# Kernel optimization log

Hardware: AMD Instinct MI355X
Metric: run time of the kernel (lower is better)

Reference implementation:

```python
import jax, jax.numpy as jnp
import numpy as np

N = 131072      # total nodes
E = 262144      # directed edges (~2 per node, molecular graphs)
B = 4096        # number of graphs
D = 300         # emb_dim
L = 5           # num_layer
MAXN = 96       # max nodes per graph (static cap)
NUM_ATOM, NUM_CHI = 120, 3
NUM_BOND, NUM_DIR = 6, 3   # bond type vocab incl. self-loop id 4; bond direction
BN_EPS = 1e-5
SELF_LOOP_BOND = 4


def setup_inputs() -> dict:
    key = jax.random.key(0)
    ks = jax.random.split(key, 24)
    s = 1.0 / np.sqrt(D)
    x = jnp.stack([jax.random.randint(ks[0], (N,), 0, NUM_ATOM),
                   jax.random.randint(ks[1], (N,), 0, NUM_CHI)], axis=1)
    edge_index = jax.random.randint(ks[2], (2, E), 0, N)
    edge_attr = jnp.stack([jax.random.randint(ks[3], (E,), 0, 4),
                           jax.random.randint(ks[4], (E,), 0, NUM_DIR)], axis=1)
    batch = jnp.sort(jax.random.randint(ks[5], (N,), 0, B)).at[-1].set(B - 1)
    return dict(
        x=x, edge_index=edge_index, edge_attr=edge_attr, batch=batch, max_nodes=MAXN,
        atom_emb1=jax.random.normal(ks[6], (NUM_ATOM, D)) * s,
        atom_emb2=jax.random.normal(ks[7], (NUM_CHI, D)) * s,
        edge_emb1=jax.random.normal(ks[8], (L, NUM_BOND, D)) * s,
        edge_emb2=jax.random.normal(ks[9], (L, NUM_DIR, D)) * s,
        W1=jax.random.normal(ks[10], (L, D, 2 * D)) * s,
        b1=jnp.zeros((L, 2 * D)),
        W2=jax.random.normal(ks[11], (L, 2 * D, D)) * (1.0 / np.sqrt(2 * D)),
        b2=jnp.zeros((L, D)),
        bn_gamma=jax.random.uniform(ks[12], (L, D), minval=0.8, maxval=1.2),
        bn_beta=jax.random.normal(ks[13], (L, D)) * 0.05,
        bn_mean=jax.random.normal(ks[14], (L, D)) * 0.05,
        bn_var=jax.random.uniform(ks[15], (L, D), minval=0.5, maxval=1.5),
    )


def reference(x, edge_index, edge_attr, batch, max_nodes,
              atom_emb1, atom_emb2, edge_emb1, edge_emb2,
              W1, b1, W2, b2, bn_gamma, bn_beta, bn_mean, bn_var):
    n = x.shape[0]
    # add self-loops with edge_attr [SELF_LOOP_BOND, 0] (chem GIN convention)
    loops = jnp.arange(n, dtype=edge_index.dtype)
    src = jnp.concatenate([edge_index[0], loops])
    dst = jnp.concatenate([edge_index[1], loops])
    sl = jnp.stack([jnp.full((n,), SELF_LOOP_BOND, edge_attr.dtype),
                    jnp.zeros((n,), edge_attr.dtype)], axis=1)
    ea = jnp.concatenate([edge_attr, sl], axis=0)

    h = atom_emb1[x[:, 0]] + atom_emb2[x[:, 1]]  # [N, D]
    for l in range(L):
        e = edge_emb1[l][ea[:, 0]] + edge_emb2[l][ea[:, 1]]     # [E+N, D]
        msg = h[src] + e                                         # gather + add
        agg = jax.ops.segment_sum(msg, dst, num_segments=n)      # scatter-add
        h = jnp.maximum(agg @ W1[l] + b1[l], 0.0) @ W2[l] + b2[l]  # GIN MLP
        h = bn_gamma[l] * (h - bn_mean[l]) * jax.lax.rsqrt(bn_var[l] + BN_EPS) + bn_beta[l]
        if l < L - 1:
            h = jnp.maximum(h, 0.0)

    # ragged -> dense pack (replaces the per-graph python copy loop)
    counts = jax.ops.segment_sum(jnp.ones((n,), jnp.int32), batch, num_segments=B)
    offsets = jnp.concatenate([jnp.zeros((1,), counts.dtype), jnp.cumsum(counts)[:-1]])
    pos = jnp.arange(n, dtype=counts.dtype) - offsets[batch]     # within-graph index
    padded = jnp.zeros((B, max_nodes, h.shape[1]), h.dtype).at[batch, pos].set(h)
    padding_mask = jnp.arange(max_nodes)[None, :] >= counts[:, None]
    return padded, padding_mask
```

## Files before the change

kernel.cpp:

```cpp
#include <hip/hip_runtime.h>

typedef _Float16 f16;
typedef __attribute__((ext_vector_type(8))) _Float16 f16x8;
typedef __attribute__((ext_vector_type(4))) float f32x4;

#define D_      300
#define DP      320
#define L_      5
#define MAXN_   96
#define NGRAPH  4096
#define MAXDEG  32

__global__ void k_prep_w(const float* __restrict__ W1, const float* __restrict__ W2,
                         f16* __restrict__ W1t, f16* __restrict__ W2t) {
  const int T1 = L_ * 640 * 320;
  const int T2 = L_ * 304 * 640;
  for (int idx = blockIdx.x * blockDim.x + threadIdx.x; idx < T1 + T2;
       idx += gridDim.x * blockDim.x) {
    if (idx < T1) {
      int l = idx / (640 * 320), r = idx % (640 * 320);
      int j = r / 320, k = r % 320;
      W1t[idx] = (j < 600 && k < 300) ? (f16)W1[(l * 300 + k) * 600 + j] : (f16)0.0f;
    } else {
      int i2 = idx - T1;
      int l = i2 / (304 * 640), r = i2 % (304 * 640);
      int c = r / 640, k = r % 640;
      W2t[i2] = (c < 300 && k < 600) ? (f16)W2[(l * 600 + k) * 300 + c] : (f16)0.0f;
    }
  }
}

__global__ void k_prep_eemb(const float* __restrict__ ee1, const float* __restrict__ ee2,
                            float* __restrict__ eemb) {
  int total = L_ * 13 * 304;
  for (int idx = blockIdx.x * blockDim.x + threadIdx.x; idx < total;
       idx += gridDim.x * blockDim.x) {
    int l = idx / (13 * 304), r = idx % (13 * 304);
    int c = r / 304, d = r % 304;
    int bond = (c == 12) ? 4 : (c / 3);
    int dir  = (c == 12) ? 0 : (c % 3);
    eemb[idx] = (d < 300) ? ee1[(l * 6 + bond) * 300 + d] + ee2[(l * 3 + dir) * 300 + d]
                          : 0.0f;
  }
}

__global__ void k_bc_init(int* counts, int* offsets) {
  int i = blockIdx.x * blockDim.x + threadIdx.x;
  if (i < NGRAPH) { counts[i] = 0; offsets[i] = 0x7fffffff; }
}
__global__ void k_zero_i32(int* p, int n) {
  for (int i = blockIdx.x * blockDim.x + threadIdx.x; i < n; i += gridDim.x * blockDim.x)
    p[i] = 0;
}
__global__ void k_bc_count(const int* __restrict__ batch, int n, int* counts, int* offsets) {
  int i = blockIdx.x * blockDim.x + threadIdx.x;
  if (i < n) { int b = batch[i]; atomicAdd(&counts[b], 1); atomicMin(&offsets[b], i); }
}
__global__ void k_pos(const int* __restrict__ batch, const int* __restrict__ offsets,
                      int n, int* __restrict__ pos) {
  int i = blockIdx.x * blockDim.x + threadIdx.x;
  if (i < n) pos[i] = i - offsets[batch[i]];
}
__global__ void k_mask(const int* __restrict__ counts, float* __restrict__ mask) {
  int i = blockIdx.x * blockDim.x + threadIdx.x;
  if (i < NGRAPH * MAXN_) {
    int b = i / MAXN_, j = i % MAXN_;
    mask[i] = (j >= counts[b]) ? 1.0f : 0.0f;
  }
}
__global__ void k_zero(uint4* __restrict__ p, long nchunks) {
  for (long i = blockIdx.x * (long)blockDim.x + threadIdx.x; i < nchunks;
       i += (long)gridDim.x * blockDim.x)
    p[i] = make_uint4(0u, 0u, 0u, 0u);
}

__global__ void k_epack(const int* __restrict__ src, const int* __restrict__ dst,
                        const int* __restrict__ ea, int ne,
                        int* __restrict__ deg, int* __restrict__ epack) {
  int e = blockIdx.x * blockDim.x + threadIdx.x;
  if (e < ne) {
    int t = dst[e];
    int p = atomicAdd(&deg[t], 1);
    if (p < MAXDEG) epack[t * MAXDEG + p] = src[e] | ((ea[2 * e] * 3 + ea[2 * e + 1]) << 17);
  }
}

__global__ void k_init_h(const int* __restrict__ x, const float* __restrict__ ae1,
                         const float* __restrict__ ae2, f16* __restrict__ h, int n) {
  long total = (long)n * DP;
  for (long idx = blockIdx.x * (long)blockDim.x + threadIdx.x; idx < total;
       idx += (long)gridDim.x * blockDim.x) {
    int i = idx / DP, d = idx % DP;
    if (d < 300) {
      int a1 = x[2 * i], a2 = x[2 * i + 1];
      h[idx] = (f16)(ae1[a1 * 300 + d] + ae2[a2 * 300 + d]);
    } else h[idx] = (f16)0.0f;
  }
}

__launch_bounds__(512)
__global__ void k_gather(const f16* __restrict__ hin, f16* __restrict__ agg,
                         const int* __restrict__ deg, const int* __restrict__ epack,
                         const float* __restrict__ em, int n) {
  int w = threadIdx.x >> 6, lane = threadIdx.x & 63;
  int node = blockIdx.x * 8 + w;
  if (node >= n) return;
  float acc[5];
  const float* ems = em + 12 * 304;
#pragma unroll
  for (int k = 0; k < 5; k++) {
    int d = lane + 64 * k;
    acc[k] = (d < 300) ? (float)hin[node * DP + d] + ems[d] : 0.0f;
  }
  int dg = deg[node]; if (dg > MAXDEG) dg = MAXDEG;
  for (int j = 0; j < dg; j++) {
    int v = epack[node * MAXDEG + j];
    int s = v & 0x1FFFF, c = v >> 17;
    const f16* hr = hin + s * DP;
    const float* er = em + c * 304;
#pragma unroll
    for (int k = 0; k < 5; k++) {
      int d = lane + 64 * k;
      if (d < 300) acc[k] += (float)hr[d] + er[d];
    }
  }
#pragma unroll
  for (int k = 0; k < 5; k++) {
    int d = lane + 64 * k;
    agg[node * DP + d] = (f16)((d < 300) ? acc[k] : 0.0f);
  }
}

template<int LAST>
__launch_bounds__(512)
__global__ void k_mlp(const f16* agg,
                      f16* hout,
                      const f16* __restrict__ W1t,
                      const f16* __restrict__ W2t,
                      const float* __restrict__ b1, const float* __restrict__ b2,
                      const float* __restrict__ bng, const float* __restrict__ bnb,
                      const float* __restrict__ bnm, const float* __restrict__ bnv,
                      float* __restrict__ outp, const int* __restrict__ batch,
                      const int* __restrict__ pos) {
  __shared__ __align__(16) unsigned char smem[122880];
  f16* As = (f16*)smem;
  f16* Hs = (f16*)(smem + 40960);
  f16* Os = (f16*)smem;

  const int tid = threadIdx.x, w = tid >> 6, lane = tid & 63;
  const int lr = lane & 15, lk = lane >> 4;
  const int n0 = blockIdx.x * 64;

#pragma unroll
  for (int q = 0; q < 5; q++) {
    int c = q * 512 + tid;
    int row = c / 40, cc = c % 40;
    f16x8 v = *(const f16x8*)(agg + (size_t)(n0 + row) * DP + cc * 8);
    *(f16x8*)(As + row * 320 + ((cc ^ (row & 7)) << 3)) = v;
  }
  __syncthreads();

#pragma unroll
  for (int j = 0; j < 5; j++) {
    const int ct = w + 8 * j;
    const int col = ct * 16 + lr;
    f32x4 a1[4] = {};
#pragma unroll
    for (int ks = 0; ks < 10; ks++) {
      int kc = ks * 4 + lk;
      f16x8 bf = *(const f16x8*)(W1t + (size_t)col * 320 + kc * 8);
#pragma unroll
      for (int rg = 0; rg < 4; rg++) {
        int row = rg * 16 + lr;
        f16x8 af = *(const f16x8*)(As + row * 320 + ((kc ^ (row & 7)) << 3));
        a1[rg] = __builtin_amdgcn_mfma_f32_16x16x32_f16(af, bf, a1[rg], 0, 0, 0);
      }
    }
    float bv = (col < 600) ? b1[col] : 0.0f;
    int chq = col >> 3, cof = col & 7;
#pragma unroll
    for (int rg = 0; rg < 4; rg++)
#pragma unroll
      for (int i = 0; i < 4; i++) {
        int row = rg * 16 + lk * 4 + i;
        Hs[row * 640 + (((chq ^ (row & 7)) << 3) | cof)] =
            (f16)fmaxf(a1[rg][i] + bv, 0.0f);
      }
  }
  __syncthreads();

#pragma unroll
  for (int j = 0; j < 3; j++) {
    const int ct = w + 8 * j;
    if (ct < 19) {
      const int col = ct * 16 + lr;
      f32x4 c2[4] = {};
#pragma unroll
      for (int ks = 0; ks < 20; ks++) {
        int kc = ks * 4 + lk;
        f16x8 bf = *(const f16x8*)(W2t + (size_t)col * 640 + kc * 8);
#pragma unroll
        for (int rg = 0; rg < 4; rg++) {
          int row = rg * 16 + lr;
          f16x8 hf = *(const f16x8*)(Hs + row * 640 + ((kc ^ (row & 7)) << 3));
          c2[rg] = __builtin_amdgcn_mfma_f32_16x16x32_f16(hf, bf, c2[rg], 0, 0, 0);
        }
      }
      bool real = col < 300;
      float b2v = real ? b2[col] : 0.0f;
      float sc  = real ? bng[col] * rsqrtf(bnv[col] + 1e-5f) : 0.0f;
      float mu  = real ? bnm[col] : 0.0f;
      float be  = real ? bnb[col] : 0.0f;
      int chq = col >> 3, cof = col & 7;
#pragma unroll
      for (int rg = 0; rg < 4; rg++)
#pragma unroll
        for (int i = 0; i < 4; i++) {
          int row = rg * 16 + lk * 4 + i;
          float v = (c2[rg][i] + b2v - mu) * sc + be;
          if (!LAST) v = fmaxf(v, 0.0f);
          Os[row * 320 + (((chq ^ (row & 7)) << 3) | cof)] =
              real ? (f16)v : (f16)0.0f;
        }
    }
  }

  if (tid < 128) {
    int row = tid >> 1, cc = 38 + (tid & 1);
    f16x8 zz = {};
    *(f16x8*)(Os + row * 320 + ((cc ^ (row & 7)) << 3)) = zz;
  }
  __syncthreads();

  if (!LAST) {
#pragma unroll
    for (int q = 0; q < 5; q++) {
      int c = q * 512 + tid;
      int row = c / 40, cc = c % 40;
      *(f16x8*)(hout + (size_t)(n0 + row) * DP + cc * 8) =
          *(const f16x8*)(Os + row * 320 + ((cc ^ (row & 7)) << 3));
    }
  } else {
    for (int idx = tid; idx < 64 * 75; idx += 512) {
      int row = idx / 75, c4 = idx % 75;
      int node = n0 + row;
      int g = batch[node], p = pos[node];
      if (p < MAXN_) {
        int col = c4 * 4;
        const f16* s = Os + row * 320 + (((col >> 3) ^ (row & 7)) << 3) + (col & 7);
        float4 v = make_float4((float)s[0], (float)s[1], (float)s[2], (float)s[3]);
        *(float4*)(outp + ((long)g * MAXN_ + p) * 300 + col) = v;
      }
    }
  }
}

extern "C" void kernel_launch(void* const* d_in, const int* in_sizes, int n_in,
                              void* d_out, int out_size, void* d_ws, size_t ws_size,
                              hipStream_t stream) {
  const int* x     = (const int*)d_in[0];
  const int* ei    = (const int*)d_in[1];
  const int* ea    = (const int*)d_in[2];
  const int* batch = (const int*)d_in[3];
  const float* ae1 = (const float*)d_in[5];
  const float* ae2 = (const float*)d_in[6];
  const float* ee1 = (const float*)d_in[7];
  const float* ee2 = (const float*)d_in[8];
  const float* W1  = (const float*)d_in[9];
  const float* b1  = (const float*)d_in[10];
  const float* W2  = (const float*)d_in[11];
  const float* b2  = (const float*)d_in[12];
  const float* bng = (const float*)d_in[13];
  const float* bnb = (const float*)d_in[14];
  const float* bnm = (const float*)d_in[15];
  const float* bnv = (const float*)d_in[16];

  const int N = in_sizes[3];
  const int E = in_sizes[2] / 2;

  char* ws = (char*)d_ws;
  f16*   hX    = (f16*)ws;
  f16*   hY    = (f16*)(ws + 83886080);
  f16*   W1t   = (f16*)(ws + 167772160);
  f16*   W2t   = (f16*)(ws + 169820160);
  float* eemb  = (float*)(ws + 171765760);
  int*   epack = (int*)(ws + 171844800);
  int*   deg   = (int*)(ws + 188622016);
  int*   pos   = (int*)(ws + 189146304);
  int*   counts= (int*)(ws + 189670592);
  int*   offs  = (int*)(ws + 189686976);

  float* outp  = (float*)d_out;
  float* maskp = outp + (long)NGRAPH * MAXN_ * D_;

  hipLaunchKernelGGL(k_prep_w, dim3(2048), dim3(256), 0, stream, W1, W2, W1t, W2t);
  hipLaunchKernelGGL(k_prep_eemb, dim3(80), dim3(256), 0, stream, ee1, ee2, eemb);
  hipLaunchKernelGGL(k_bc_init, dim3(16), dim3(256), 0, stream, counts, offs);
  hipLaunchKernelGGL(k_zero_i32, dim3(512), dim3(256), 0, stream, deg, N);
  hipLaunchKernelGGL(k_bc_count, dim3((N + 255) / 256), dim3(256), 0, stream, batch, N, counts, offs);
  hipLaunchKernelGGL(k_pos, dim3((N + 255) / 256), dim3(256), 0, stream, batch, offs, N, pos);
  hipLaunchKernelGGL(k_mask, dim3((NGRAPH * MAXN_ + 255) / 256), dim3(256), 0, stream, counts, maskp);
  hipLaunchKernelGGL(k_epack, dim3((E + 255) / 256), dim3(256), 0, stream,
                     ei, ei + E, ea, E, deg, epack);
  hipLaunchKernelGGL(k_zero, dim3(4096), dim3(256), 0, stream,
                     (uint4*)outp, (long)NGRAPH * MAXN_ * D_ / 4);
  hipLaunchKernelGGL(k_init_h, dim3(8192), dim3(256), 0, stream, x, ae1, ae2, hX, N);

  for (int l = 0; l < L_; l++) {
    const f16* hi = (l & 1) ? hY : hX;
    f16*       ag = (l & 1) ? hX : hY;
    hipLaunchKernelGGL(k_gather, dim3(N / 8), dim3(512), 0, stream,
                       hi, ag, deg, epack, eemb + l * 13 * 304, N);
    if (l < L_ - 1)
      hipLaunchKernelGGL((k_mlp<0>), dim3(N / 64), dim3(512), 0, stream,
                         ag, ag,
                         W1t + l * 640 * 320, W2t + l * 304 * 640,
                         b1 + l * 600, b2 + l * 300,
                         bng + l * 300, bnb + l * 300, bnm + l * 300, bnv + l * 300,
                         outp, batch, pos);
    else
      hipLaunchKernelGGL((k_mlp<1>), dim3(N / 64), dim3(512), 0, stream,
                         ag, ag,
                         W1t + l * 640 * 320, W2t + l * 304 * 640,
                         b1 + l * 600, b2 + l * 300,
                         bng + l * 300, bnb + l * 300, bnm + l * 300, bnv + l * 300,
                         outp, batch, pos);
  }
}
```

Measured before the change: 1.738 ms.

## Split MLP hidden dimension into two halves to shrink LDS and double occupancy

The fused GIN MLP kernel now computes the 640-wide hidden layer in two 320-column halves. Each half is fed straight into the second GEMM, which accumulates in registers, so the hidden buffer in LDS shrinks from 64x640 to 64x320 and total LDS drops from 120KB to 80KB. Launch bounds request two blocks per CU, so MFMA work can overlap with memory and sync latency. In exchange each thread holds more accumulator registers, which the launch-bounds cap may force into spills, and there is an extra barrier. The last-layer output read from LDS is also vectorised to a single 4-wide f16 load.

```diff
diff --git a/kernel.cpp b/kernel.cpp
--- a/kernel.cpp
+++ b/kernel.cpp
@@ -2,6 +2,7 @@
 
 typedef _Float16 f16;
 typedef __attribute__((ext_vector_type(8))) _Float16 f16x8;
+typedef __attribute__((ext_vector_type(4))) _Float16 f16x4;
 typedef __attribute__((ext_vector_type(4))) float f32x4;
 
 #define D_      300
@@ -132,7 +133,7 @@
 }
 
 template<int LAST>
-__launch_bounds__(512)
+__launch_bounds__(512, 2)
 __global__ void k_mlp(const f16* agg,
                       f16* hout,
                       const f16* __restrict__ W1t,
@@ -142,7 +143,7 @@
                       const float* __restrict__ bnm, const float* __restrict__ bnv,
                       float* __restrict__ outp, const int* __restrict__ batch,
                       const int* __restrict__ pos) {
-  __shared__ __align__(16) unsigned char smem[122880];
+  __shared__ __align__(16) unsigned char smem[81920];
   f16* As = (f16*)smem;
   f16* Hs = (f16*)(smem + 40960);
   f16* Os = (f16*)smem;
@@ -160,52 +161,66 @@
   }
   __syncthreads();
 
-#pragma unroll
-  for (int j = 0; j < 5; j++) {
-    const int ct = w + 8 * j;
-    const int col = ct * 16 + lr;
-    f32x4 a1[4] = {};
-#pragma unroll
-    for (int ks = 0; ks < 10; ks++) {
-      int kc = ks * 4 + lk;
-      f16x8 bf = *(const f16x8*)(W1t + (size_t)col * 320 + kc * 8);
-#pragma unroll
-      for (int rg = 0; rg < 4; rg++) {
-        int row = rg * 16 + lr;
-        f16x8 af = *(const f16x8*)(As + row * 320 + ((kc ^ (row & 7)) << 3));
-        a1[rg] = __builtin_amdgcn_mfma_f32_16x16x32_f16(af, bf, a1[rg], 0, 0, 0);
+  f32x4 cacc[3][4] = {};
+
+#pragma unroll
+  for (int h = 0; h < 2; h++) {
+    if (h) __syncthreads();
+#pragma unroll
+    for (int j = 0; j < 3; j++) {
+      const int ct = w + 8 * j;
+      if (ct < 20) {
+        const int colg = h * 320 + ct * 16 + lr;
+        f32x4 a1[4] = {};
+#pragma unroll
+        for (int ks = 0; ks < 10; ks++) {
+          f16x8 bf = *(const f16x8*)(W1t + (size_t)colg * 320 + ks * 32 + lk * 8);
+          int kc = ks * 4 + lk;
+#pragma unroll
+          for (int rg = 0; rg < 4; rg++) {
+            int row = rg * 16 + lr;
+            f16x8 af = *(const f16x8*)(As + row * 320 + ((kc ^ (row & 7)) << 3));
+            a1[rg] = __builtin_amdgcn_mfma_f32_16x16x32_f16(af, bf, a1[rg], 0, 0, 0);
+          }
+        }
+        float bv = (colg < 600) ? b1[colg] : 0.0f;
+        int chq = (ct * 16 + lr) >> 3, cof = lr & 7;
+#pragma unroll
+        for (int rg = 0; rg < 4; rg++)
+#pragma unroll
+          for (int i = 0; i < 4; i++) {
+            int row = rg * 16 + lk * 4 + i;
+            Hs[row * 320 + (((chq ^ (row & 7)) << 3) | cof)] =
+                (f16)fmaxf(a1[rg][i] + bv, 0.0f);
+          }
       }
     }
-    float bv = (col < 600) ? b1[col] : 0.0f;
-    int chq = col >> 3, cof = col & 7;
-#pragma unroll
-    for (int rg = 0; rg < 4; rg++)
-#pragma unroll
-      for (int i = 0; i < 4; i++) {
-        int row = rg * 16 + lk * 4 + i;
-        Hs[row * 640 + (((chq ^ (row & 7)) << 3) | cof)] =
-            (f16)fmaxf(a1[rg][i] + bv, 0.0f);
+    __syncthreads();
+#pragma unroll
+    for (int j = 0; j < 3; j++) {
+      const int ct = w + 8 * j;
+      if (ct < 19) {
+        const int col = ct * 16 + lr;
+#pragma unroll
+        for (int ks = 0; ks < 10; ks++) {
+          f16x8 bf = *(const f16x8*)(W2t + (size_t)col * 640 + h * 320 + ks * 32 + lk * 8);
+          int kc = ks * 4 + lk;
+#pragma unroll
+          for (int rg = 0; rg < 4; rg++) {
+            int row = rg * 16 + lr;
+            f16x8 hf = *(const f16x8*)(Hs + row * 320 + ((kc ^ (row & 7)) << 3));
+            cacc[j][rg] = __builtin_amdgcn_mfma_f32_16x16x32_f16(hf, bf, cacc[j][rg], 0, 0, 0);
+          }
+        }
       }
-  }
-  __syncthreads();
+    }
+  }
 
 #pragma unroll
   for (int j = 0; j < 3; j++) {
     const int ct = w + 8 * j;
     if (ct < 19) {
       const int col = ct * 16 + lr;
-      f32x4 c2[4] = {};
-#pragma unroll
-      for (int ks = 0; ks < 20; ks++) {
-        int kc = ks * 4 + lk;
-        f16x8 bf = *(const f16x8*)(W2t + (size_t)col * 640 + kc * 8);
-#pragma unroll
-        for (int rg = 0; rg < 4; rg++) {
-          int row = rg * 16 + lr;
-          f16x8 hf = *(const f16x8*)(Hs + row * 640 + ((kc ^ (row & 7)) << 3));
-          c2[rg] = __builtin_amdgcn_mfma_f32_16x16x32_f16(hf, bf, c2[rg], 0, 0, 0);
-        }
-      }
       bool real = col < 300;
       float b2v = real ? b2[col] : 0.0f;
       float sc  = real ? bng[col] * rsqrtf(bnv[col] + 1e-5f) : 0.0f;
@@ -217,7 +232,7 @@
 #pragma unroll
         for (int i = 0; i < 4; i++) {
           int row = rg * 16 + lk * 4 + i;
-          float v = (c2[rg][i] + b2v - mu) * sc + be;
+          float v = (cacc[j][rg][i] + b2v - mu) * sc + be;
           if (!LAST) v = fmaxf(v, 0.0f);
           Os[row * 320 + (((chq ^ (row & 7)) << 3) | cof)] =
               real ? (f16)v : (f16)0.0f;
@@ -248,7 +263,8 @@
       if (p < MAXN_) {
         int col = c4 * 4;
         const f16* s = Os + row * 320 + (((col >> 3) ^ (row & 7)) << 3) + (col & 7);
-        float4 v = make_float4((float)s[0], (float)s[1], (float)s[2], (float)s[3]);
+        f16x4 hv = *(const f16x4*)s;
+        float4 v = make_float4((float)hv[0], (float)hv[1], (float)hv[2], (float)hv[3]);
         *(float4*)(outp + ((long)g * MAXN_ + p) * 300 + col) = v;
       }
     }
```

Result: slower. 2.314 ms (+33.1%).

## Fuse edge gather-aggregation into GIN MLP kernel prologue

Applied to the files above, without the earlier changes.

Removes the separate gather kernel and performs neighbor aggregation directly into shared memory inside the MLP kernel, with 8 threads per node handling pairs of features. This avoids writing and re-reading the aggregated tensor through global memory and drops one launch per layer. The gather now runs with fewer lanes per node and higher register pressure (38 accumulators per thread), which may reduce memory-level parallelism for the random row loads. Also vectorizes the final output read from shared memory.

```diff
diff --git a/kernel.cpp b/kernel.cpp
--- a/kernel.cpp
+++ b/kernel.cpp
@@ -2,6 +2,8 @@
 
 typedef _Float16 f16;
 typedef __attribute__((ext_vector_type(8))) _Float16 f16x8;
+typedef __attribute__((ext_vector_type(4))) _Float16 f16x4;
+typedef __attribute__((ext_vector_type(2))) _Float16 f16x2;
 typedef __attribute__((ext_vector_type(4))) float f32x4;
 
 #define D_      300
@@ -98,43 +100,12 @@
   }
 }
 
-__launch_bounds__(512)
-__global__ void k_gather(const f16* __restrict__ hin, f16* __restrict__ agg,
-                         const int* __restrict__ deg, const int* __restrict__ epack,
-                         const float* __restrict__ em, int n) {
-  int w = threadIdx.x >> 6, lane = threadIdx.x & 63;
-  int node = blockIdx.x * 8 + w;
-  if (node >= n) return;
-  float acc[5];
-  const float* ems = em + 12 * 304;
-#pragma unroll
-  for (int k = 0; k < 5; k++) {
-    int d = lane + 64 * k;
-    acc[k] = (d < 300) ? (float)hin[node * DP + d] + ems[d] : 0.0f;
-  }
-  int dg = deg[node]; if (dg > MAXDEG) dg = MAXDEG;
-  for (int j = 0; j < dg; j++) {
-    int v = epack[node * MAXDEG + j];
-    int s = v & 0x1FFFF, c = v >> 17;
-    const f16* hr = hin + s * DP;
-    const float* er = em + c * 304;
-#pragma unroll
-    for (int k = 0; k < 5; k++) {
-      int d = lane + 64 * k;
-      if (d < 300) acc[k] += (float)hr[d] + er[d];
-    }
-  }
-#pragma unroll
-  for (int k = 0; k < 5; k++) {
-    int d = lane + 64 * k;
-    agg[node * DP + d] = (f16)((d < 300) ? acc[k] : 0.0f);
-  }
-}
-
 template<int LAST>
 __launch_bounds__(512)
-__global__ void k_mlp(const f16* agg,
-                      f16* hout,
+__global__ void k_mlp(const f16* __restrict__ hin,
+                      f16* __restrict__ hout,
+                      const int* __restrict__ deg, const int* __restrict__ epack,
+                      const float* __restrict__ em,
                       const f16* __restrict__ W1t,
                       const f16* __restrict__ W2t,
                       const float* __restrict__ b1, const float* __restrict__ b2,
@@ -151,12 +122,46 @@
   const int lr = lane & 15, lk = lane >> 4;
   const int n0 = blockIdx.x * 64;
 
-#pragma unroll
-  for (int q = 0; q < 5; q++) {
-    int c = q * 512 + tid;
-    int row = c / 40, cc = c % 40;
-    f16x8 v = *(const f16x8*)(agg + (size_t)(n0 + row) * DP + cc * 8);
-    *(f16x8*)(As + row * 320 + ((cc ^ (row & 7)) << 3)) = v;
+  {
+    const int ln = tid >> 3, sub = tid & 7;
+    const int node = n0 + ln;
+    const float* ems = em + 12 * 304;
+    float accx[19], accy[19];
+#pragma unroll
+    for (int k = 0; k < 19; k++) {
+      int d = (sub << 1) + (k << 4);
+      if (d < 300) {
+        f16x2 hv = *(const f16x2*)(hin + (size_t)node * DP + d);
+        accx[k] = (float)hv[0] + ems[d];
+        accy[k] = (float)hv[1] + ems[d + 1];
+      } else { accx[k] = 0.0f; accy[k] = 0.0f; }
+    }
+    int dg = deg[node]; if (dg > MAXDEG) dg = MAXDEG;
+    for (int j = 0; j < dg; j++) {
+      int v = epack[node * MAXDEG + j];
+      int s = v & 0x1FFFF, c = v >> 17;
+      const f16* hr = hin + (size_t)s * DP;
+      const float* er = em + c * 304;
+#pragma unroll
+      for (int k = 0; k < 19; k++) {
+        int d = (sub << 1) + (k << 4);
+        if (d < 300) {
+          f16x2 hv = *(const f16x2*)(hr + d);
+          float2 ev = *(const float2*)(er + d);
+          accx[k] += (float)hv[0] + ev.x;
+          accy[k] += (float)hv[1] + ev.y;
+        }
+      }
+    }
+#pragma unroll
+    for (int k = 0; k < 20; k++) {
+      int d = (sub << 1) + (k << 4);
+      f16x2 o;
+      if (k < 19 && d < 300) { o[0] = (f16)accx[k]; o[1] = (f16)accy[k]; }
+      else { o[0] = (f16)0.0f; o[1] = (f16)0.0f; }
+      int chunk = d >> 3;
+      *(f16x2*)(As + ln * 320 + ((chunk ^ (ln & 7)) << 3) + (d & 7)) = o;
+    }
   }
   __syncthreads();
 
@@ -168,7 +173,7 @@
 #pragma unroll
     for (int ks = 0; ks < 10; ks++) {
       int kc = ks * 4 + lk;
-      f16x8 bf = *(const f16x8*)(W1t + (size_t)col * 320 + kc * 8);
+      f16x8 bf = *(const f16x8*)(W1t + (size_t)col * 320 + ks * 32 + lk * 8);
 #pragma unroll
       for (int rg = 0; rg < 4; rg++) {
         int row = rg * 16 + lr;
@@ -198,7 +203,7 @@
 #pragma unroll
       for (int ks = 0; ks < 20; ks++) {
         int kc = ks * 4 + lk;
-        f16x8 bf = *(const f16x8*)(W2t + (size_t)col * 640 + kc * 8);
+        f16x8 bf = *(const f16x8*)(W2t + (size_t)col * 640 + ks * 32 + lk * 8);
 #pragma unroll
         for (int rg = 0; rg < 4; rg++) {
           int row = rg * 16 + lr;
@@ -248,7 +253,8 @@
       if (p < MAXN_) {
         int col = c4 * 4;
         const f16* s = Os + row * 320 + (((col >> 3) ^ (row & 7)) << 3) + (col & 7);
-        float4 v = make_float4((float)s[0], (float)s[1], (float)s[2], (float)s[3]);
+        f16x4 hv = *(const f16x4*)s;
+        float4 v = make_float4((float)hv[0], (float)hv[1], (float)hv[2], (float)hv[3]);
         *(float4*)(outp + ((long)g * MAXN_ + p) * 300 + col) = v;
       }
     }
@@ -308,19 +314,17 @@
 
   for (int l = 0; l < L_; l++) {
     const f16* hi = (l & 1) ? hY : hX;
-    f16*       ag = (l & 1) ? hX : hY;
-    hipLaunchKernelGGL(k_gather, dim3(N / 8), dim3(512), 0, stream,
-                       hi, ag, deg, epack, eemb + l * 13 * 304, N);
+    f16*       ho = (l & 1) ? hX : hY;
     if (l < L_ - 1)
       hipLaunchKernelGGL((k_mlp<0>), dim3(N / 64), dim3(512), 0, stream,
-                         ag, ag,
+                         hi, ho, deg, epack, eemb + l * 13 * 304,
                          W1t + l * 640 * 320, W2t + l * 304 * 640,
                          b1 + l * 600, b2 + l * 300,
                          bng + l * 300, bnb + l * 300, bnm + l * 300, bnv + l * 300,
                          outp, batch, pos);
     else
       hipLaunchKernelGGL((k_mlp<1>), dim3(N / 64), dim3(512), 0, stream,
-                         ag, ag,
+                         hi, ho, deg, epack, eemb + l * 13 * 304,
                          W1t + l * 640 * 320, W2t + l * 304 * 640,
                          b1 + l * 600, b2 + l * 300,
                          bng + l * 300, bnb + l * 300, bnm + l * 300, bnv + l * 300,
```

After: 1.847 ms. 6.2% more time.

## Use 32x32x16 MFMA tiles in GIN MLP and zero only padded output rows

Applied to the files above, without the earlier changes.

Switches both MLP GEMMs from 16x16x32 to 32x32x16 MFMA instructions. Each wave now computes a 64x32 output tile, which halves the per-wave B-fragment global loads and changes the K-step and accumulator layout. W2t is padded to 320 columns so the second GEMM covers the pad columns and the explicit pad-zeroing step can go. The output zero fill now writes only the padded positions instead of the whole dense tensor, and the final write reads four halves as one vector load. Work is split unevenly now: the first GEMM has 20 column tiles over 8 waves, so some waves run 3 tiles and others 2, which risks idle waves.

```diff
diff --git a/kernel.cpp b/kernel.cpp
--- a/kernel.cpp
+++ b/kernel.cpp
@@ -2,7 +2,9 @@
 
 typedef _Float16 f16;
 typedef __attribute__((ext_vector_type(8))) _Float16 f16x8;
+typedef __attribute__((ext_vector_type(4))) _Float16 f16x4;
 typedef __attribute__((ext_vector_type(4))) float f32x4;
+typedef __attribute__((ext_vector_type(16))) float f32x16;
 
 #define D_      300
 #define DP      320
@@ -14,7 +16,7 @@
 __global__ void k_prep_w(const float* __restrict__ W1, const float* __restrict__ W2,
                          f16* __restrict__ W1t, f16* __restrict__ W2t) {
   const int T1 = L_ * 640 * 320;
-  const int T2 = L_ * 304 * 640;
+  const int T2 = L_ * 320 * 640;
   for (int idx = blockIdx.x * blockDim.x + threadIdx.x; idx < T1 + T2;
        idx += gridDim.x * blockDim.x) {
     if (idx < T1) {
@@ -23,7 +25,7 @@
       W1t[idx] = (j < 600 && k < 300) ? (f16)W1[(l * 300 + k) * 600 + j] : (f16)0.0f;
     } else {
       int i2 = idx - T1;
-      int l = i2 / (304 * 640), r = i2 % (304 * 640);
+      int l = i2 / (320 * 640), r = i2 % (320 * 640);
       int c = r / 640, k = r % 640;
       W2t[i2] = (c < 300 && k < 600) ? (f16)W2[(l * 600 + k) * 300 + c] : (f16)0.0f;
     }
@@ -68,10 +70,16 @@
     mask[i] = (j >= counts[b]) ? 1.0f : 0.0f;
   }
 }
-__global__ void k_zero(uint4* __restrict__ p, long nchunks) {
-  for (long i = blockIdx.x * (long)blockDim.x + threadIdx.x; i < nchunks;
-       i += (long)gridDim.x * blockDim.x)
-    p[i] = make_uint4(0u, 0u, 0u, 0u);
+__global__ void k_zero_pad(const int* __restrict__ counts, float* __restrict__ outp) {
+  long total = (long)NGRAPH * MAXN_ * 75;
+  for (long idx = blockIdx.x * (long)blockDim.x + threadIdx.x; idx < total;
+       idx += (long)gridDim.x * blockDim.x) {
+    long r = idx / 75;
+    int c4 = (int)(idx % 75);
+    int g = (int)(r / MAXN_), p = (int)(r % MAXN_);
+    if (p >= counts[g])
+      *(float4*)(outp + r * 300 + c4 * 4) = make_float4(0.f, 0.f, 0.f, 0.f);
+  }
 }
 
 __global__ void k_epack(const int* __restrict__ src, const int* __restrict__ dst,
@@ -148,7 +156,7 @@
   f16* Os = (f16*)smem;
 
   const int tid = threadIdx.x, w = tid >> 6, lane = tid & 63;
-  const int lr = lane & 15, lk = lane >> 4;
+  const int l31 = lane & 31, lk2 = lane >> 5;
   const int n0 = blockIdx.x * 64;
 
 #pragma unroll
@@ -161,50 +169,51 @@
   __syncthreads();
 
 #pragma unroll
-  for (int j = 0; j < 5; j++) {
-    const int ct = w + 8 * j;
-    const int col = ct * 16 + lr;
-    f32x4 a1[4] = {};
-#pragma unroll
-    for (int ks = 0; ks < 10; ks++) {
-      int kc = ks * 4 + lk;
-      f16x8 bf = *(const f16x8*)(W1t + (size_t)col * 320 + kc * 8);
-#pragma unroll
-      for (int rg = 0; rg < 4; rg++) {
-        int row = rg * 16 + lr;
-        f16x8 af = *(const f16x8*)(As + row * 320 + ((kc ^ (row & 7)) << 3));
-        a1[rg] = __builtin_amdgcn_mfma_f32_16x16x32_f16(af, bf, a1[rg], 0, 0, 0);
-      }
-    }
-    float bv = (col < 600) ? b1[col] : 0.0f;
-    int chq = col >> 3, cof = col & 7;
-#pragma unroll
-    for (int rg = 0; rg < 4; rg++)
-#pragma unroll
-      for (int i = 0; i < 4; i++) {
-        int row = rg * 16 + lk * 4 + i;
-        Hs[row * 640 + (((chq ^ (row & 7)) << 3) | cof)] =
-            (f16)fmaxf(a1[rg][i] + bv, 0.0f);
-      }
-  }
-  __syncthreads();
-
-#pragma unroll
   for (int j = 0; j < 3; j++) {
     const int ct = w + 8 * j;
-    if (ct < 19) {
-      const int col = ct * 16 + lr;
-      f32x4 c2[4] = {};
+    if (ct < 20) {
+      const int col = ct * 32 + l31;
+      f32x16 acc0 = {}, acc1 = {};
+      const int r0 = l31, r1 = 32 + l31;
 #pragma unroll
       for (int ks = 0; ks < 20; ks++) {
-        int kc = ks * 4 + lk;
-        f16x8 bf = *(const f16x8*)(W2t + (size_t)col * 640 + kc * 8);
-#pragma unroll
-        for (int rg = 0; rg < 4; rg++) {
-          int row = rg * 16 + lr;
-          f16x8 hf = *(const f16x8*)(Hs + row * 640 + ((kc ^ (row & 7)) << 3));
-          c2[rg] = __builtin_amdgcn_mfma_f32_16x16x32_f16(hf, bf, c2[rg], 0, 0, 0);
-        }
+        f16x8 bf = *(const f16x8*)(W1t + (size_t)col * 320 + ks * 16 + lk2 * 8);
+        int kc = ks * 2 + lk2;
+        f16x8 a0 = *(const f16x8*)(As + r0 * 320 + ((kc ^ (r0 & 7)) << 3));
+        f16x8 a1v = *(const f16x8*)(As + r1 * 320 + ((kc ^ (r1 & 7)) << 3));
+        acc0 = __builtin_amdgcn_mfma_f32_32x32x16_f16(a0, bf, acc0, 0, 0, 0);
+        acc1 = __builtin_amdgcn_mfma_f32_32x32x16_f16(a1v, bf, acc1, 0, 0, 0);
+      }
+      float bv = (col < 600) ? b1[col] : 0.0f;
+      int chq = col >> 3, cof = col & 7;
+#pragma unroll
+      for (int r = 0; r < 16; r++) {
+        int rowl = (r & 3) + 8 * (r >> 2) + 4 * lk2;
+        int row0 = rowl, row1 = 32 + rowl;
+        Hs[row0 * 640 + (((chq ^ (row0 & 7)) << 3) | cof)] =
+            (f16)fmaxf(acc0[r] + bv, 0.0f);
+        Hs[row1 * 640 + (((chq ^ (row1 & 7)) << 3) | cof)] =
+            (f16)fmaxf(acc1[r] + bv, 0.0f);
+      }
+    }
+  }
+  __syncthreads();
+
+#pragma unroll
+  for (int j = 0; j < 2; j++) {
+    const int ct = w + 8 * j;
+    if (ct < 10) {
+      const int col = ct * 32 + l31;
+      f32x16 acc0 = {}, acc1 = {};
+      const int r0 = l31, r1 = 32 + l31;
+#pragma unroll
+      for (int ks = 0; ks < 40; ks++) {
+        f16x8 bf = *(const f16x8*)(W2t + (size_t)col * 640 + ks * 16 + lk2 * 8);
+        int kc = ks * 2 + lk2;
+        f16x8 h0 = *(const f16x8*)(Hs + r0 * 640 + ((kc ^ (r0 & 7)) << 3));
+        f16x8 h1 = *(const f16x8*)(Hs + r1 * 640 + ((kc ^ (r1 & 7)) << 3));
+        acc0 = __builtin_amdgcn_mfma_f32_32x32x16_f16(h0, bf, acc0, 0, 0, 0);
+        acc1 = __builtin_amdgcn_mfma_f32_32x32x16_f16(h1, bf, acc1, 0, 0, 0);
       }
       bool real = col < 300;
       float b2v = real ? b2[col] : 0.0f;
@@ -213,22 +222,16 @@
       float be  = real ? bnb[col] : 0.0f;
       int chq = col >> 3, cof = col & 7;
 #pragma unroll
-      for (int rg = 0; rg < 4; rg++)
-#pragma unroll
-        for (int i = 0; i < 4; i++) {
-          int row = rg * 16 + lk * 4 + i;
-          float v = (c2[rg][i] + b2v - mu) * sc + be;
-          if (!LAST) v = fmaxf(v, 0.0f);
-          Os[row * 320 + (((chq ^ (row & 7)) << 3) | cof)] =
-              real ? (f16)v : (f16)0.0f;
-        }
-    }
-  }
-
-  if (tid < 128) {
-    int row = tid >> 1, cc = 38 + (tid & 1);
-    f16x8 zz = {};
-    *(f16x8*)(Os + row * 320 + ((cc ^ (row & 7)) << 3)) = zz;
+      for (int r = 0; r < 16; r++) {
+        int rowl = (r & 3) + 8 * (r >> 2) + 4 * lk2;
+        int row0 = rowl, row1 = 32 + rowl;
+        float v0 = (acc0[r] + b2v - mu) * sc + be;
+        float v1 = (acc1[r] + b2v - mu) * sc + be;
+        if (!LAST) { v0 = fmaxf(v0, 0.0f); v1 = fmaxf(v1, 0.0f); }
+        Os[row0 * 320 + (((chq ^ (row0 & 7)) << 3) | cof)] = real ? (f16)v0 : (f16)0.0f;
+        Os[row1 * 320 + (((chq ^ (row1 & 7)) << 3) | cof)] = real ? (f16)v1 : (f16)0.0f;
+      }
+    }
   }
   __syncthreads();
 
@@ -248,7 +251,8 @@
       if (p < MAXN_) {
         int col = c4 * 4;
         const f16* s = Os + row * 320 + (((col >> 3) ^ (row & 7)) << 3) + (col & 7);
-        float4 v = make_float4((float)s[0], (float)s[1], (float)s[2], (float)s[3]);
+        f16x4 hv = *(const f16x4*)s;
+        float4 v = make_float4((float)hv[0], (float)hv[1], (float)hv[2], (float)hv[3]);
         *(float4*)(outp + ((long)g * MAXN_ + p) * 300 + col) = v;
       }
     }
@@ -283,12 +287,12 @@
   f16*   hY    = (f16*)(ws + 83886080);
   f16*   W1t   = (f16*)(ws + 167772160);
   f16*   W2t   = (f16*)(ws + 169820160);
-  float* eemb  = (float*)(ws + 171765760);
-  int*   epack = (int*)(ws + 171844800);
-  int*   deg   = (int*)(ws + 188622016);
-  int*   pos   = (int*)(ws + 189146304);
-  int*   counts= (int*)(ws + 189670592);
-  int*   offs  = (int*)(ws + 189686976);
+  float* eemb  = (float*)(ws + 171868160);
+  int*   epack = (int*)(ws + 171947200);
+  int*   deg   = (int*)(ws + 188724416);
+  int*   pos   = (int*)(ws + 189248704);
+  int*   counts= (int*)(ws + 189772992);
+  int*   offs  = (int*)(ws + 189789376);
 
   float* outp  = (float*)d_out;
   float* maskp = outp + (long)NGRAPH * MAXN_ * D_;
@@ -302,8 +306,7 @@
   hipLaunchKernelGGL(k_mask, dim3((NGRAPH * MAXN_ + 255) / 256), dim3(256), 0, stream, counts, maskp);
   hipLaunchKernelGGL(k_epack, dim3((E + 255) / 256), dim3(256), 0, stream,
                      ei, ei + E, ea, E, deg, epack);
-  hipLaunchKernelGGL(k_zero, dim3(4096), dim3(256), 0, stream,
-                     (uint4*)outp, (long)NGRAPH * MAXN_ * D_ / 4);
+  hipLaunchKernelGGL(k_zero_pad, dim3(4096), dim3(256), 0, stream, counts, outp);
   hipLaunchKernelGGL(k_init_h, dim3(8192), dim3(256), 0, stream, x, ae1, ae2, hX, N);
 
   for (int l = 0; l < L_; l++) {
@@ -314,14 +317,14 @@
     if (l < L_ - 1)
       hipLaunchKernelGGL((k_mlp<0>), dim3(N / 64), dim3(512), 0, stream,
                          ag, ag,
-                         W1t + l * 640 * 320, W2t + l * 304 * 640,
+                         W1t + l * 640 * 320, W2t + l * 320 * 640,
                          b1 + l * 600, b2 + l * 300,
                          bng + l * 300, bnb + l * 300, bnm + l * 300, bnv + l * 300,
                          outp, batch, pos);
     else
       hipLaunchKernelGGL((k_mlp<1>), dim3(N / 64), dim3(512), 0, stream,
                          ag, ag,
-                         W1t + l * 640 * 320, W2t + l * 304 * 640,
+                         W1t + l * 640 * 320, W2t + l * 320 * 640,
                          b1 + l * 600, b2 + l * 300,
                          bng + l * 300, bnb + l * 300, bnm + l * 300, bnv + l * 300,
                          outp, batch, pos);
```

After: 1.888 ms. 8.6% more time.
